# Kernel tuning notes

Measured on AMD Instinct MI355X. Metric: run time of the kernel, lower is better.

The kernel has to match this reference:

```python
import jax, jax.numpy as jnp
import numpy as np

EMBED_DIM = 512
VIR_HEADS = 8


def _make_buffers():
    # angle: 1/10000**linspace(0,1,embed//H//2), each entry repeated twice (rotary pairs)
    half = EMBED_DIM // VIR_HEADS // 2
    angle = 1.0 / 10000 ** jnp.linspace(0.0, 1.0, half)
    angle = jnp.repeat(angle, 2)  # [head_dim]
    decay = jnp.log(1 - 2 ** (-2 - 5 * jnp.arange(VIR_HEADS, dtype=jnp.float32) / VIR_HEADS))
    return angle.astype(jnp.float32), decay.astype(jnp.float32)


def setup_inputs() -> dict:
    key = jax.random.key(0)
    B, H, N1, N2 = 8, 8, 32, 32
    offsets = jax.random.normal(key, (B, H, N1, N2, 2), dtype=jnp.float32)
    angle, decay = _make_buffers()
    return {"slen": N1 * N2, "offsets": offsets, "angle": angle, "decay": decay}


def reference(slen, offsets, angle, decay):
    B, H, N1, N2, _ = offsets.shape
    idx1 = jnp.arange(N1, dtype=offsets.dtype)
    idx2 = jnp.arange(N2, dtype=offsets.dtype)

    # key-side rotary phases: index_k[i*N2+j] = i + j
    index_k = (idx1[:, None] + idx2[None, :]).reshape(slen)  # [slen]
    phase_k = index_k[:, None] * angle[None, :]               # [slen, D]
    sin_k, cos_k = jnp.sin(phase_k), jnp.cos(phase_k)

    # query-side deformed indices
    index1_q = idx1.reshape(1, 1, N1, 1) + offsets[..., 0]    # [B,H,N1,N2]
    index2_q = idx2.reshape(1, 1, 1, N2) + offsets[..., 1]    # [B,H,N1,N2]
    index_q = (index1_q + index2_q).reshape(B, H, slen, 1)    # [B,H,slen,1]
    phase_q = index_q * angle.reshape(1, 1, 1, -1)            # [B,H,slen,D]
    sin_q, cos_q = jnp.sin(phase_q), jnp.cos(phase_q)

    # L1 distance between deformed query position and each key grid position
    d1 = jnp.abs(index1_q[..., None, None] - idx1.reshape(1, 1, 1, 1, N1, 1))  # [B,H,N1,N2,N1,1]
    d2 = jnp.abs(index2_q[..., None, None] - idx2.reshape(1, 1, 1, 1, 1, N2))  # [B,H,N1,N2,1,N2]
    mask = (d1 + d2).reshape(B, H, slen, slen)
    mask = jnp.exp(mask * decay[None, :, None, None])
    mask = jnp.nan_to_num(mask)
    mask = mask / jnp.sqrt(jnp.sum(mask, axis=-1, keepdims=True))
    return sin_q, cos_q, sin_k, cos_k, mask
```

## Files before the change

kernel.cpp:

```cpp
#include <hip/hip_runtime.h>
#include <math.h>

#define OFF_COSQ  4194304
#define OFF_SINK  8388608
#define OFF_COSK  8454144
#define OFF_MASK  8519680
#define NROWS     65536

typedef float floatx4 __attribute__((ext_vector_type(4)));

__global__ __launch_bounds__(256) void retnet_fused_kernel(
    const float* __restrict__ offsets,
    const float* __restrict__ angle,
    const float* __restrict__ decay,
    float* __restrict__ out)
{
    const int wave = blockIdx.x * 4 + (threadIdx.x >> 6);
    const int lane = threadIdx.x & 63;
    if (wave >= NROWS) return;

    const int bh = wave >> 10;
    const int s  = wave & 1023;
    const int h  = bh & 7;
    const int i  = s >> 5;
    const int j  = s & 31;

    const float off0 = offsets[(wave << 1) + 0];
    const float off1 = offsets[(wave << 1) + 1];
    const float i1q  = (float)i + off0;
    const float i2q  = (float)j + off1;
    const float dec  = decay[h];
    const float ang  = angle[lane];

    {
        float sq, cq;
        __sincosf((i1q + i2q) * ang, &sq, &cq);
        __builtin_nontemporal_store(sq, &out[(size_t)wave * 64 + lane]);
        __builtin_nontemporal_store(cq, &out[OFF_COSQ + (size_t)wave * 64 + lane]);
    }

    if (bh == 0) {
        float sk, ck;
        __sincosf((float)(i + j) * ang, &sk, &ck);
        __builtin_nontemporal_store(sk, &out[OFF_SINK + (size_t)s * 64 + lane]);
        __builtin_nontemporal_store(ck, &out[OFF_COSK + (size_t)s * 64 + lane]);
    }

    float v;
    if (lane < 32) v = __expf(dec * fabsf(i1q - (float)lane));
    else           v = __expf(dec * fabsf(i2q - (float)(lane - 32)));

    float sum = v;
    #pragma unroll
    for (int m = 16; m >= 1; m >>= 1) sum += __shfl_xor(sum, m, 64);
    const float sum1 = __shfl(sum, 0, 64);
    const float sum2 = __shfl(sum, 32, 64);
    const float invnorm = rsqrtf(sum1 * sum2);

    const int jj0 = (lane & 7) * 4;
    float e2a[4];
    #pragma unroll
    for (int c = 0; c < 4; ++c)
        e2a[c] = __expf(dec * fabsf(i2q - (float)(jj0 + c))) * invnorm;

    floatx4* mrow = (floatx4*)(out + OFF_MASK + (size_t)wave * 1024);
    #pragma unroll
    for (int k = 0; k < 4; ++k) {
        const int ii = k * 8 + (lane >> 3);
        const float e1 = __expf(dec * fabsf(i1q - (float)ii));
        floatx4 r;
        r.x = e1 * e2a[0];
        r.y = e1 * e2a[1];
        r.z = e1 * e2a[2];
        r.w = e1 * e2a[3];
        __builtin_nontemporal_store(r, &mrow[k * 64 + lane]);
    }
}

extern "C" void kernel_launch(void* const* d_in, const int* in_sizes, int n_in,
                              void* d_out, int out_size, void* d_ws, size_t ws_size,
                              hipStream_t stream) {
    const float* offsets = (const float*)d_in[1];
    const float* angle   = (const float*)d_in[2];
    const float* decay   = (const float*)d_in[3];
    float* out = (float*)d_out;

    const int blocks = NROWS / 4;
    retnet_fused_kernel<<<blocks, 256, 0, stream>>>(offsets, angle, decay, out);
}
```

Measured before the change: 300.3 us.

## Split fused kernel into prep pass writing normalized factors and mask-store pass

The single kernel becomes two. The first computes the sin/cos outputs and the per-row separable exponential factors (the first half pre-scaled by the inverse norm) and writes them to a workspace. The second reads those factors and writes the outer-product mask rows. This removes redundant exp evaluations in the store-heavy pass, at the cost of a second launch and an extra workspace write and read.

```diff
diff --git a/kernel.cpp b/kernel.cpp
--- a/kernel.cpp
+++ b/kernel.cpp
@@ -9,15 +9,15 @@
 
 typedef float floatx4 __attribute__((ext_vector_type(4)));
 
-__global__ __launch_bounds__(256) void retnet_fused_kernel(
+__global__ __launch_bounds__(256) void retnet_prep_kernel(
     const float* __restrict__ offsets,
     const float* __restrict__ angle,
     const float* __restrict__ decay,
-    float* __restrict__ out)
+    float* __restrict__ out,
+    float* __restrict__ ws)
 {
     const int wave = blockIdx.x * 4 + (threadIdx.x >> 6);
     const int lane = threadIdx.x & 63;
-    if (wave >= NROWS) return;
 
     const int bh = wave >> 10;
     const int s  = wave & 1023;
@@ -57,22 +57,30 @@
     const float sum2 = __shfl(sum, 32, 64);
     const float invnorm = rsqrtf(sum1 * sum2);
 
+    ws[(size_t)wave * 64 + lane] = (lane < 32) ? v * invnorm : v;
+}
+
+__global__ __launch_bounds__(256) void retnet_mask_kernel(
+    const float* __restrict__ ws,
+    float* __restrict__ out)
+{
+    const int wave = blockIdx.x * 4 + (threadIdx.x >> 6);
+    const int lane = threadIdx.x & 63;
+
+    const float* row = ws + (size_t)wave * 64;
+
     const int jj0 = (lane & 7) * 4;
-    float e2a[4];
+    const floatx4 e2q = *(const floatx4*)(row + 32 + jj0);
+
+    const int ii0 = lane >> 3;
+    float e1a[4];
     #pragma unroll
-    for (int c = 0; c < 4; ++c)
-        e2a[c] = __expf(dec * fabsf(i2q - (float)(jj0 + c))) * invnorm;
+    for (int k = 0; k < 4; ++k) e1a[k] = row[k * 8 + ii0];
 
     floatx4* mrow = (floatx4*)(out + OFF_MASK + (size_t)wave * 1024);
     #pragma unroll
     for (int k = 0; k < 4; ++k) {
-        const int ii = k * 8 + (lane >> 3);
-        const float e1 = __expf(dec * fabsf(i1q - (float)ii));
-        floatx4 r;
-        r.x = e1 * e2a[0];
-        r.y = e1 * e2a[1];
-        r.z = e1 * e2a[2];
-        r.w = e1 * e2a[3];
+        floatx4 r = e2q * e1a[k];
         __builtin_nontemporal_store(r, &mrow[k * 64 + lane]);
     }
 }
@@ -84,7 +92,9 @@
     const float* angle   = (const float*)d_in[2];
     const float* decay   = (const float*)d_in[3];
     float* out = (float*)d_out;
+    float* ws  = (float*)d_ws;
 
     const int blocks = NROWS / 4;
-    retnet_fused_kernel<<<blocks, 256, 0, stream>>>(offsets, angle, decay, out);
+    retnet_prep_kernel<<<blocks, 256, 0, stream>>>(offsets, angle, decay, out, ws);
+    retnet_mask_kernel<<<blocks, 256, 0, stream>>>(ws, out);
 }
```

Measured after the change: 308.2 us. +2.6%, slower.
